# Kernel optimization log

Hardware: AMD Instinct MI355X
Metric: run time of the kernel (lower is better)

Reference implementation:

```python
import jax, jax.numpy as jnp
import numpy as np

B, T_DEC, T_ENC = 64, 128, 256
D_X, N_HIDDEN, N_FEED = 1024, 1024, 1024


def _glorot(key, shape):
    fan_in = shape[0]
    return jax.random.normal(key, shape, dtype=jnp.float32) / np.sqrt(fan_in)


def setup_inputs() -> dict:
    key = jax.random.key(0)
    ks = jax.random.split(key, 10)
    H = N_HIDDEN
    return {
        "x": jax.random.normal(ks[0], (B, T_DEC, D_X), dtype=jnp.float32),
        "o_enc": jax.random.normal(ks[1], (B, T_ENC, H), dtype=jnp.float32),
        "h_enc": jax.random.normal(ks[2], (B, H), dtype=jnp.float32),
        # input-feeding FFN: Dense(n_feed, tanh), input dim = n_hidden
        "Wfeed": _glorot(ks[3], (H, N_FEED)),
        "bfeed": jnp.zeros((N_FEED,), dtype=jnp.float32),
        # GRU (keras v2, reset_after=True): kernel [n_feed+d_x, 3H], recurrent [H, 3H]
        "Wx": _glorot(ks[4], (N_FEED + D_X, 3 * H)),
        "Wh": _glorot(ks[5], (H, 3 * H)),
        "bxi": jnp.zeros((3 * H,), dtype=jnp.float32),  # input bias
        "bhr": jnp.zeros((3 * H,), dtype=jnp.float32),  # recurrent bias (reset_after)
        # attention FFN: Dense(n_hidden, tanh), input dim = 2H (concat[value, h_dec])
        "Watt": _glorot(ks[6], (2 * H, H)),
        "batt": jnp.zeros((H,), dtype=jnp.float32),
    }


def reference(x, o_enc, h_enc, Wfeed, bfeed, Wx, Wh, bxi, bhr, Watt, batt):
    # x: [B, T_dec, d_x], o_enc: [B, T_enc, H], h_enc: [B, H]
    def step(carry, x_t):
        h, i_feed = carry  # h: [B,H] GRU state, i_feed: [B,H] previous attention output
        # input feeding FFN + concat with current token
        i_cat = jnp.concatenate([jnp.tanh(i_feed @ Wfeed + bfeed), x_t], axis=-1)
        # GRU cell (keras reset_after=True semantics)
        gx = i_cat @ Wx + bxi  # [B, 3H]
        gh = h @ Wh + bhr      # [B, 3H]
        xz, xr, xh = jnp.split(gx, 3, axis=-1)
        hz, hr, hh = jnp.split(gh, 3, axis=-1)
        z = jax.nn.sigmoid(xz + hz)
        r = jax.nn.sigmoid(xr + hr)
        hcand = jnp.tanh(xh + r * hh)
        h_new = z * h + (1.0 - z) * hcand  # [B, H]
        # Luong dot attention over encoder outputs
        scores = jnp.einsum('bh,bth->bt', h_new, o_enc)       # [B, T_enc]
        attn = jax.nn.softmax(scores, axis=-1)
        value = jnp.einsum('bt,bth->bh', attn, o_enc)         # [B, H]
        h_att = jnp.tanh(jnp.concatenate([value, h_new], axis=-1) @ Watt + batt)
        return (h_new, h_att), h_att

    i_feed0 = jnp.zeros_like(h_enc)
    x_t_major = jnp.swapaxes(x, 0, 1)  # [T_dec, B, d_x]
    _, outs = jax.lax.scan(step, (h_enc, i_feed0), x_t_major)
    return jnp.swapaxes(outs, 0, 1)  # [B, T_dec, H]
```

## Files before the change

### kernel.cpp

```cpp
#include <hip/hip_runtime.h>
#include <hip/hip_bf16.h>


#define NWG 256
#define NTHR 1024
constexpr int BB = 64, TD = 128, TE = 256, HH = 1024, H3 = 3072;

typedef __attribute__((ext_vector_type(8))) __bf16 bf16x8;
typedef __attribute__((ext_vector_type(4))) float f32x4;
using bf = __hip_bfloat16;

__device__ __forceinline__ f32x4 mfma16(bf16x8 a, bf16x8 b, f32x4 c) {
  return __builtin_amdgcn_mfma_f32_16x16x32_bf16(a, b, c, 0, 0, 0);
}

struct Args {
  const float *x, *o_enc, *bfeed, *bxi, *bhr, *batt;
  const bf *Wf0, *Wf1, *Wf2, *Wh0, *Wh1, *Wh2;
  const bf *WxF0, *WxF1, *WxF2, *WxX0, *WxX1, *WxX2, *Wa0, *Wa1, *Wa2;
  float *h_f32;
  float *gx;
  float *gh, *scores;
  bf *hs0, *hs1, *hs2, *ff0, *ff1, *ff2, *ifd0, *ifd1, *ifd2;
  bf *xt0, *xt1, *xt2, *vl0, *vl1, *vl2;
  unsigned *cnt, *cnt2, *go, *afl;
  float *out;
};

__device__ __forceinline__ void gbar(unsigned ep, const Args& a, int wg) {
  __syncthreads();
  if (threadIdx.x == 0) {
    __threadfence();
    unsigned* sub = a.cnt + (wg & 15) * 32;
    unsigned o = __hip_atomic_fetch_add(sub, 1u, __ATOMIC_ACQ_REL, __HIP_MEMORY_SCOPE_AGENT);
    if (o == 15) {
      __hip_atomic_store(sub, 0u, __ATOMIC_RELAXED, __HIP_MEMORY_SCOPE_AGENT);
      unsigned o2 = __hip_atomic_fetch_add(a.cnt2, 1u, __ATOMIC_ACQ_REL, __HIP_MEMORY_SCOPE_AGENT);
      if (o2 == 15) {
        __hip_atomic_store(a.cnt2, 0u, __ATOMIC_RELAXED, __HIP_MEMORY_SCOPE_AGENT);
        __hip_atomic_store(a.go, ep, __ATOMIC_RELEASE, __HIP_MEMORY_SCOPE_AGENT);
      }
    }
    while (__hip_atomic_load(a.go, __ATOMIC_RELAXED, __HIP_MEMORY_SCOPE_AGENT) < ep)
      __builtin_amdgcn_s_sleep(2);
    __threadfence();
  }
  __syncthreads();
}

__device__ __forceinline__ void split3_write(bf* p0, bf* p1, bf* p2, size_t i, float v) {
  bf b0 = __float2bfloat16(v);
  float r1 = v - __bfloat162float(b0);
  bf b1 = __float2bfloat16(r1);
  float r2 = r1 - __bfloat162float(b1);
  p0[i] = b0; p1[i] = b1; p2[i] = __float2bfloat16(r2);
}

template <int K>
__device__ __forceinline__ f32x4 gemm6(const bf* A0, const bf* A1, const bf* A2,
                                       const bf* B0, const bf* B1, const bf* B2) {
  f32x4 c0 = {0.f, 0.f, 0.f, 0.f}, c1 = c0, c2 = c0, c3 = c0;
  bf16x8 a0 = *(const bf16x8*)(A0);
  bf16x8 a1 = *(const bf16x8*)(A1);
  bf16x8 a2 = *(const bf16x8*)(A2);
  bf16x8 b0 = *(const bf16x8*)(B0);
  bf16x8 b1 = *(const bf16x8*)(B1);
  bf16x8 b2 = *(const bf16x8*)(B2);
#pragma unroll
  for (int k = 0; k < K; k += 32) {
    bf16x8 na0, na1, na2, nb0, nb1, nb2;
    if (k + 32 < K) {
      na0 = *(const bf16x8*)(A0 + k + 32);
      na1 = *(const bf16x8*)(A1 + k + 32);
      na2 = *(const bf16x8*)(A2 + k + 32);
      nb0 = *(const bf16x8*)(B0 + k + 32);
      nb1 = *(const bf16x8*)(B1 + k + 32);
      nb2 = *(const bf16x8*)(B2 + k + 32);
    }
    c0 = mfma16(a0, b0, c0);
    c1 = mfma16(a0, b1, c1);
    c2 = mfma16(a1, b0, c2);
    c3 = mfma16(a1, b1, c3);
    c0 = mfma16(a0, b2, c0);
    c1 = mfma16(a2, b0, c1);
    if (k + 32 < K) {
      a0 = na0; a1 = na1; a2 = na2;
      b0 = nb0; b1 = nb1; b2 = nb2;
    }
  }
  f32x4 s;
#pragma unroll
  for (int i = 0; i < 4; ++i) s[i] = (c0[i] + c1[i]) + (c2[i] + c3[i]);
  return s;
}

__global__ __launch_bounds__(NTHR, 4) void decoder_main(Args a) {
  const int wg = blockIdx.x;
  const int tid = threadIdx.x;
  const int lane = tid & 63;
  const int wv = tid >> 6;
  const int lrow = lane & 15;
  const int lkg = lane >> 4;

  __shared__ float s_u[4096];
  __shared__ float s_h[HH];
  __shared__ float s_sm[TE];
  __shared__ float s_red[8];
  __shared__ float s_val[2][256];
  __shared__ int s_idx[TE];
  __shared__ int s_wcnt[4];

  unsigned ep = 0;

  for (int t = 0; t < TD; ++t) {
    {
      const bool isf = (wg < 64);
      const int j0 = (isf ? wg : wg - 64) * 16;
      const bf* A0 = isf ? a.ifd0 : a.hs0;
      const bf* A1 = isf ? a.ifd1 : a.hs1;
      const bf* A2 = isf ? a.ifd2 : a.hs2;
      const bf* B0 = isf ? a.Wf0 : a.Wh0;
      const bf* B1 = isf ? a.Wf1 : a.Wh1;
      const bf* B2 = isf ? a.Wf2 : a.Wh2;
      const int mt = wv >> 2, kq = wv & 3;
      const size_t aoff = (size_t)(mt * 16 + lrow) * HH + kq * 256 + lkg * 8;
      const size_t boff = (size_t)(j0 + lrow) * HH + kq * 256 + lkg * 8;
      f32x4 acc = gemm6<256>(A0 + aoff, A1 + aoff, A2 + aoff, B0 + boff, B1 + boff, B2 + boff);
#pragma unroll
      for (int r = 0; r < 4; ++r) s_u[kq * 1024 + mt * 256 + (lkg * 4 + r) * 16 + lrow] = acc[r];
      __syncthreads();
      {
        const int row = tid >> 4, c = tid & 15;
        const int emt = row >> 4, r2 = row & 15;
        const int e = emt * 256 + r2 * 16 + c;
        float v = (s_u[e] + s_u[1024 + e]) + (s_u[2048 + e] + s_u[3072 + e]);
        const int col = j0 + c;
        if (isf) {
          float f = tanhf(v + a.bfeed[col]);
          split3_write(a.ff0, a.ff1, a.ff2, (size_t)row * HH + col, f);
        } else {
          a.gh[(size_t)row * H3 + col] = v + a.bhr[col];
        }
      }
    }
    gbar(++ep, a, wg);

    {
      const int xcd = wg & 7, slot = wg >> 3;
      const int jt = xcd * 8 + (slot >> 2), sub = slot & 3;
      if (wv < 12) {
        const int ci = wv >> 2, ku = wv & 3;
        const int c2 = sub * 3 + ci;
        const int g = c2 >> 2, mt = c2 & 3;
        const int op = ku >> 1, kh = ku & 1;
        const bf* A0 = op ? a.xt0 : a.ff0;
        const bf* A1 = op ? a.xt1 : a.ff1;
        const bf* A2 = op ? a.xt2 : a.ff2;
        const bf* B0 = op ? a.WxX0 : a.WxF0;
        const bf* B1 = op ? a.WxX1 : a.WxF1;
        const bf* B2 = op ? a.WxX2 : a.WxF2;
        const size_t aoff = (size_t)(mt * 16 + lrow) * HH + kh * 512 + lkg * 8;
        const size_t boff = (size_t)(g * HH + jt * 16 + lrow) * HH + kh * 512 + lkg * 8;
        f32x4 acc = gemm6<512>(A0 + aoff, A1 + aoff, A2 + aoff, B0 + boff, B1 + boff, B2 + boff);
#pragma unroll
        for (int r = 0; r < 4; ++r)
          s_u[ci * 1024 + ku * 256 + (lkg * 4 + r) * 16 + lrow] = acc[r];
      }
      __syncthreads();
      if (tid < 768) {
        const int ci2 = tid >> 8, e = tid & 255;
        const int r16 = e >> 4, c16 = e & 15;
        const int base = ci2 * 1024 + e;
        float v = (s_u[base] + s_u[base + 256]) + (s_u[base + 512] + s_u[base + 768]);
        const int c2 = sub * 3 + ci2;
        const int g = c2 >> 2, mt = c2 & 3;
        a.gx[(size_t)(mt * 16 + r16) * H3 + g * 1024 + jt * 16 + c16] = v;
      }
    }
    gbar(++ep, a, wg);

    {
      const int b = wg & 63, q = wg >> 6;
      const float* hold = a.h_f32 + (size_t)(t & 1) * (BB * HH);
      float* hnew = a.h_f32 + (size_t)((t + 1) & 1) * (BB * HH);
      const float* ghb = a.gh + (size_t)b * H3;
      {
        const int col = tid;
        const float* gxb = a.gx + (size_t)b * H3;
        float gz = a.bxi[col] + gxb[col];
        float gr = a.bxi[HH + col] + gxb[HH + col];
        float gc = a.bxi[2 * HH + col] + gxb[2 * HH + col];
        float z = 1.f / (1.f + expf(-(gz + ghb[col])));
        float rr = 1.f / (1.f + expf(-(gr + ghb[HH + col])));
        float hc = tanhf(gc + rr * ghb[2 * HH + col]);
        float hn = z * hold[(size_t)b * HH + col] + (1.f - z) * hc;
        s_h[col] = hn;
        if (q == 0) {
          hnew[(size_t)b * HH + col] = hn;
          split3_write(a.hs0, a.hs1, a.hs2, (size_t)b * HH + col, hn);
        }
      }
      __syncthreads();
      {
        f32x4 sh0 = *(const f32x4*)(s_h + 0 + lane * 4);
        f32x4 sh1 = *(const f32x4*)(s_h + 256 + lane * 4);
        f32x4 sh2 = *(const f32x4*)(s_h + 512 + lane * 4);
        f32x4 sh3 = *(const f32x4*)(s_h + 768 + lane * 4);
        const float* obase = a.o_enc + ((size_t)b * TE + q * 64 + wv * 4) * HH + lane * 4;
        f32x4 o0 = *(const f32x4*)(obase);
        f32x4 o1 = *(const f32x4*)(obase + 256);
        f32x4 o2 = *(const f32x4*)(obase + 512);
        f32x4 o3 = *(const f32x4*)(obase + 768);
#pragma unroll
        for (int i = 0; i < 4; ++i) {
          f32x4 n0, n1, n2, n3;
          if (i + 1 < 4) {
            const float* nr = obase + (size_t)(i + 1) * HH;
            n0 = *(const f32x4*)(nr);
            n1 = *(const f32x4*)(nr + 256);
            n2 = *(const f32x4*)(nr + 512);
            n3 = *(const f32x4*)(nr + 768);
          }
          float s = o0[0] * sh0[0] + o0[1] * sh0[1] + o0[2] * sh0[2] + o0[3] * sh0[3]
                  + o1[0] * sh1[0] + o1[1] * sh1[1] + o1[2] * sh1[2] + o1[3] * sh1[3]
                  + o2[0] * sh2[0] + o2[1] * sh2[1] + o2[2] * sh2[2] + o2[3] * sh2[3]
                  + o3[0] * sh3[0] + o3[1] * sh3[1] + o3[2] * sh3[2] + o3[3] * sh3[3];
          for (int off = 32; off; off >>= 1) s += __shfl_xor(s, off);
          if (lane == 0) a.scores[(size_t)b * TE + q * 64 + wv * 4 + i] = s;
          o0 = n0; o1 = n1; o2 = n2; o3 = n3;
        }
      }
      __syncthreads();
      if (tid == 0) {
        __threadfence();
        __hip_atomic_store(&a.afl[b * 4 + q], (unsigned)(t + 1),
                           __ATOMIC_RELEASE, __HIP_MEMORY_SCOPE_AGENT);
        for (int p = 1; p < 4; ++p) {
          unsigned idx = b * 4 + ((q + p) & 3);
          while (__hip_atomic_load(&a.afl[idx], __ATOMIC_RELAXED, __HIP_MEMORY_SCOPE_AGENT)
                 < (unsigned)(t + 1))
            __builtin_amdgcn_s_sleep(1);
        }
        __threadfence();
      }
      __syncthreads();
      float sc = 0.f, p = 0.f;
      if (tid < 256) {
        sc = a.scores[(size_t)b * TE + tid];
        float v = sc;
        for (int off = 32; off; off >>= 1) v = fmaxf(v, __shfl_xor(v, off));
        if (lane == 0) s_red[wv] = v;
      }
      __syncthreads();
      {
        float mx = fmaxf(fmaxf(s_red[0], s_red[1]), fmaxf(s_red[2], s_red[3]));
        if (tid < 256) {
          p = expf(sc - mx);
          float sum = p;
          for (int off = 32; off; off >>= 1) sum += __shfl_xor(sum, off);
          if (lane == 0) s_red[4 + wv] = sum;
        }
      }
      __syncthreads();
      bool act = false;
      unsigned long long bm = 0;
      if (tid < 256) {
        float tot = s_red[4] + s_red[5] + s_red[6] + s_red[7];
        float w2 = p / tot;
        s_sm[tid] = w2;
        act = (w2 > 1e-8f);
        bm = __ballot(act);
        if (lane == 0) s_wcnt[wv] = __popcll(bm);
      }
      __syncthreads();
      if (tid < 256 && act) {
        int base = 0;
        for (int w2i = 0; w2i < wv; ++w2i) base += s_wcnt[w2i];
        int pos = base + __popcll(bm & ((1ULL << lane) - 1));
        s_idx[pos] = tid;
      }
      __syncthreads();
      const int nact = s_wcnt[0] + s_wcnt[1] + s_wcnt[2] + s_wcnt[3];
      if (tid < 512) {
        const int c = tid & 255, th = tid >> 8;
        const int j = q * 256 + c;
        const float* ob = a.o_enc + (size_t)b * TE * HH + j;
        float accv = 0.f;
        int ii = th;
        for (; ii + 6 < nact; ii += 8) {
          const int i0 = s_idx[ii], i1 = s_idx[ii + 2], i2 = s_idx[ii + 4], i3 = s_idx[ii + 6];
          const float v0 = ob[(size_t)i0 * HH];
          const float v1 = ob[(size_t)i1 * HH];
          const float v2 = ob[(size_t)i2 * HH];
          const float v3 = ob[(size_t)i3 * HH];
          accv += s_sm[i0] * v0;
          accv += s_sm[i1] * v1;
          accv += s_sm[i2] * v2;
          accv += s_sm[i3] * v3;
        }
        for (; ii < nact; ii += 2) {
          const int tt2 = s_idx[ii];
          accv += s_sm[tt2] * ob[(size_t)tt2 * HH];
        }
        s_val[th][c] = accv;
      }
      __syncthreads();
      if (tid < 256)
        split3_write(a.vl0, a.vl1, a.vl2, (size_t)b * HH + q * 256 + tid,
                     s_val[0][tid] + s_val[1][tid]);
    }
    gbar(++ep, a, wg);

    {
      const int cu = wg & 63;
      const int mt = wg >> 6;
      const int kq16 = wv;
      const bool isv = (kq16 < 8);
      const int koff = (kq16 & 7) * 128;
      const bf* A0 = isv ? a.vl0 : a.hs0;
      const bf* A1 = isv ? a.vl1 : a.hs1;
      const bf* A2 = isv ? a.vl2 : a.hs2;
      const size_t aoff = (size_t)(mt * 16 + lrow) * HH + koff + lkg * 8;
      const size_t boff = (size_t)(cu * 16 + lrow) * 2048 + kq16 * 128 + lkg * 8;
      f32x4 acc = gemm6<128>(A0 + aoff, A1 + aoff, A2 + aoff,
                             a.Wa0 + boff, a.Wa1 + boff, a.Wa2 + boff);
#pragma unroll
      for (int r = 0; r < 4; ++r)
        s_u[kq16 * 256 + (lkg * 4 + r) * 16 + lrow] = acc[r];
      __syncthreads();
      if (tid < 256) {
        const int r16 = tid >> 4, c16 = tid & 15;
        const int e = r16 * 16 + c16;
        float v = a.batt[cu * 16 + c16];
#pragma unroll
        for (int kq = 0; kq < 16; ++kq) v += s_u[kq * 256 + e];
        float hv = tanhf(v);
        const int row = mt * 16 + r16;
        const int col = cu * 16 + c16;
        a.out[((size_t)row * TD + t) * HH + col] = hv;
        split3_write(a.ifd0, a.ifd1, a.ifd2, (size_t)row * HH + col, hv);
      }
      if (wg < 64 && t + 1 < TD) {
        split3_write(a.xt0, a.xt1, a.xt2, (size_t)wg * HH + tid,
                     a.x[((size_t)wg * TD + (t + 1)) * HH + tid]);
      }
    }
    gbar(++ep, a, wg);
  }
}

__global__ void k_tr3(const float* src, bf* d0, bf* d1, bf* d2, int R, int C) {
  __shared__ float tile[32][33];
  int c0 = blockIdx.x * 32, r0 = blockIdx.y * 32;
  int tx = threadIdx.x & 31, ty = threadIdx.x >> 5;
  for (int i = ty; i < 32; i += 8)
    tile[i][tx] = src[(size_t)(r0 + i) * C + c0 + tx];
  __syncthreads();
  for (int i = ty; i < 32; i += 8) {
    float v = tile[tx][i];
    size_t o = (size_t)(c0 + i) * R + r0 + tx;
    bf b0 = __float2bfloat16(v);
    float r1 = v - __bfloat162float(b0);
    bf b1 = __float2bfloat16(r1);
    d0[o] = b0; d1[o] = b1; d2[o] = __float2bfloat16(r1 - __bfloat162float(b1));
  }
}

__global__ void k_init(const float* h_enc, float* h_f32, bf* h0, bf* h1, bf* h2,
                       bf* i0, bf* i1, bf* i2, const float* x, bf* x0, bf* x1, bf* x2) {
  int i = blockIdx.x * blockDim.x + threadIdx.x;
  float v = h_enc[i];
  h_f32[i] = v;
  split3_write(h0, h1, h2, i, v);
  bf z = __float2bfloat16(0.f);
  i0[i] = z; i1[i] = z; i2[i] = z;
  int row = i >> 10, col = i & 1023;
  split3_write(x0, x1, x2, i, x[((size_t)row * TD + 0) * HH + col]);
}

extern "C" void kernel_launch(void* const* d_in, const int* in_sizes, int n_in,
                              void* d_out, int out_size, void* d_ws, size_t ws_size,
                              hipStream_t stream) {
  const float* x     = (const float*)d_in[0];
  const float* o_enc = (const float*)d_in[1];
  const float* h_enc = (const float*)d_in[2];
  const float* Wfeed = (const float*)d_in[3];
  const float* bfeed = (const float*)d_in[4];
  const float* Wx    = (const float*)d_in[5];
  const float* Wh    = (const float*)d_in[6];
  const float* bxi   = (const float*)d_in[7];
  const float* bhr   = (const float*)d_in[8];
  const float* Watt  = (const float*)d_in[9];
  const float* batt  = (const float*)d_in[10];

  char* w = (char*)d_ws;
  auto alloc = [&](size_t b) { char* p = w; w += (b + 255) & ~255ULL; return p; };

  const size_t M1 = (size_t)1024 * 1024 * 2;
  bf* Wf[3];  for (auto& p : Wf)  p = (bf*)alloc(M1);
  bf* Wh_[3]; for (auto& p : Wh_) p = (bf*)alloc(3 * M1);
  bf* WxF[3]; for (auto& p : WxF) p = (bf*)alloc(3 * M1);
  bf* WxX[3]; for (auto& p : WxX) p = (bf*)alloc(3 * M1);
  bf* Wa[3];  for (auto& p : Wa)  p = (bf*)alloc(2 * M1);
  float* h_f32  = (float*)alloc((size_t)2 * BB * HH * 4);
  float* gx     = (float*)alloc((size_t)BB * H3 * 4);
  float* gh     = (float*)alloc((size_t)BB * H3 * 4);
  float* scores = (float*)alloc((size_t)BB * TE * 4);
  const size_t AB = (size_t)BB * HH * 2;
  bf *hs[3], *ff[3], *ifd[3], *xt[3], *vl[3];
  for (auto& p : hs)  p = (bf*)alloc(AB);
  for (auto& p : ff)  p = (bf*)alloc(AB);
  for (auto& p : ifd) p = (bf*)alloc(AB);
  for (auto& p : xt)  p = (bf*)alloc(AB);
  for (auto& p : vl)  p = (bf*)alloc(AB);
  unsigned* flags = (unsigned*)alloc(8192);

  hipMemsetAsync(flags, 0, 8192, stream);
  k_tr3<<<dim3(32, 32), 256, 0, stream>>>(Wfeed, Wf[0], Wf[1], Wf[2], 1024, 1024);
  k_tr3<<<dim3(96, 32), 256, 0, stream>>>(Wx, WxF[0], WxF[1], WxF[2], 1024, 3072);
  k_tr3<<<dim3(96, 32), 256, 0, stream>>>(Wx + (size_t)1024 * 3072, WxX[0], WxX[1], WxX[2], 1024, 3072);
  k_tr3<<<dim3(96, 32), 256, 0, stream>>>(Wh, Wh_[0], Wh_[1], Wh_[2], 1024, 3072);
  k_tr3<<<dim3(32, 64), 256, 0, stream>>>(Watt, Wa[0], Wa[1], Wa[2], 2048, 1024);
  k_init<<<BB * HH / 256, 256, 0, stream>>>(h_enc, h_f32, hs[0], hs[1], hs[2],
                                            ifd[0], ifd[1], ifd[2], x, xt[0], xt[1], xt[2]);

  Args a;
  a.x = x; a.o_enc = o_enc; a.bfeed = bfeed; a.bxi = bxi; a.bhr = bhr; a.batt = batt;
  a.Wf0 = Wf[0]; a.Wf1 = Wf[1]; a.Wf2 = Wf[2];
  a.Wh0 = Wh_[0]; a.Wh1 = Wh_[1]; a.Wh2 = Wh_[2];
  a.WxF0 = WxF[0]; a.WxF1 = WxF[1]; a.WxF2 = WxF[2];
  a.WxX0 = WxX[0]; a.WxX1 = WxX[1]; a.WxX2 = WxX[2];
  a.Wa0 = Wa[0]; a.Wa1 = Wa[1]; a.Wa2 = Wa[2];
  a.h_f32 = h_f32; a.gx = gx; a.gh = gh; a.scores = scores;
  a.hs0 = hs[0]; a.hs1 = hs[1]; a.hs2 = hs[2];
  a.ff0 = ff[0]; a.ff1 = ff[1]; a.ff2 = ff[2];
  a.ifd0 = ifd[0]; a.ifd1 = ifd[1]; a.ifd2 = ifd[2];
  a.xt0 = xt[0]; a.xt1 = xt[1]; a.xt2 = xt[2];
  a.vl0 = vl[0]; a.vl1 = vl[1]; a.vl2 = vl[2];
  a.cnt = flags; a.cnt2 = flags + 512; a.go = flags + 544; a.afl = flags + 576;
  a.out = (float*)d_out;

  decoder_main<<<NWG, NTHR, 0, stream>>>(a);
}
```

Measured before the change: 22.62 ms.

## Replace full grid barrier after feed GEMM with counter wait and per-XCD relays

The grid barrier now releases in two levels: eight leader workgroups watch the global go flag and republish it to per-XCD flags, which the remaining workgroups poll, so fewer blocks hammer one address. The full barrier after the feed/recurrent GEMM phase is replaced by a counter that only the feed-producing workgroups increment, and consumers wait until all 64 feed tiles of this step are written. The gh-producing workgroups no longer hold up the next phase at that point. This relies on gh not being read before a later barrier and on the flag buffer being large enough and zeroed at the new offsets.

```diff
diff --git a/kernel.cpp b/kernel.cpp
--- a/kernel.cpp
+++ b/kernel.cpp
@@ -23,7 +23,7 @@
   float *gh, *scores;
   bf *hs0, *hs1, *hs2, *ff0, *ff1, *ff2, *ifd0, *ifd1, *ifd2;
   bf *xt0, *xt1, *xt2, *vl0, *vl1, *vl2;
-  unsigned *cnt, *cnt2, *go, *afl;
+  unsigned *cnt, *cnt2, *go, *afl, *gox, *ffc, *ffx;
   float *out;
 };
 
@@ -41,8 +41,15 @@
         __hip_atomic_store(a.go, ep, __ATOMIC_RELEASE, __HIP_MEMORY_SCOPE_AGENT);
       }
     }
-    while (__hip_atomic_load(a.go, __ATOMIC_RELAXED, __HIP_MEMORY_SCOPE_AGENT) < ep)
-      __builtin_amdgcn_s_sleep(2);
+    if (wg < 8) {
+      while (__hip_atomic_load(a.go, __ATOMIC_RELAXED, __HIP_MEMORY_SCOPE_AGENT) < ep)
+        __builtin_amdgcn_s_sleep(1);
+      __hip_atomic_store(a.gox + wg * 32, ep, __ATOMIC_RELEASE, __HIP_MEMORY_SCOPE_AGENT);
+    } else {
+      while (__hip_atomic_load(a.gox + (wg & 7) * 32, __ATOMIC_RELAXED,
+                               __HIP_MEMORY_SCOPE_AGENT) < ep)
+        __builtin_amdgcn_s_sleep(1);
+    }
     __threadfence();
   }
   __syncthreads();
@@ -142,8 +149,26 @@
           a.gh[(size_t)row * H3 + col] = v + a.bhr[col];
         }
       }
-    }
-    gbar(++ep, a, wg);
+      __syncthreads();
+      if (isf && tid == 0) {
+        __threadfence();
+        __hip_atomic_fetch_add(a.ffc, 1u, __ATOMIC_ACQ_REL, __HIP_MEMORY_SCOPE_AGENT);
+      }
+    }
+    if (tid == 0) {
+      const unsigned tgt = 64u * (unsigned)(t + 1);
+      if (wg < 8) {
+        while (__hip_atomic_load(a.ffc, __ATOMIC_RELAXED, __HIP_MEMORY_SCOPE_AGENT) < tgt)
+          __builtin_amdgcn_s_sleep(1);
+        __hip_atomic_store(a.ffx + wg * 32, tgt, __ATOMIC_RELEASE, __HIP_MEMORY_SCOPE_AGENT);
+      } else {
+        while (__hip_atomic_load(a.ffx + (wg & 7) * 32, __ATOMIC_RELAXED,
+                                 __HIP_MEMORY_SCOPE_AGENT) < tgt)
+          __builtin_amdgcn_s_sleep(1);
+      }
+      __threadfence();
+    }
+    __syncthreads();
 
     {
       const int xcd = wg & 7, slot = wg >> 3;
@@ -438,6 +463,7 @@
   a.xt0 = xt[0]; a.xt1 = xt[1]; a.xt2 = xt[2];
   a.vl0 = vl[0]; a.vl1 = vl[1]; a.vl2 = vl[2];
   a.cnt = flags; a.cnt2 = flags + 512; a.go = flags + 544; a.afl = flags + 576;
+  a.gox = flags + 832; a.ffc = flags + 1088; a.ffx = flags + 1120;
   a.out = (float*)d_out;
 
   decoder_main<<<NWG, NTHR, 0, stream>>>(a);
```

Result: faster. 21.61 ms (-4.5%).
